# Kernel optimization log

Hardware: AMD Instinct MI355X
Metric: run time of the kernel (lower is better)

The kernel has to match this reference:

```python
import jax, jax.numpy as jnp
import numpy as np

B = 8192
DIM_Q = 1024
DIM_U = 1024
NUM_CHARTS = 16
TOP_K = 2


def setup_inputs() -> dict:
    key = jax.random.key(0)
    k1, k2, k3 = jax.random.split(key, 3)
    q = jax.random.normal(k1, (B, DIM_Q), dtype=jnp.float32)
    weights = jax.random.uniform(k2, (B, NUM_CHARTS), dtype=jnp.float32)
    # W_stack init: -I + 0.01*randn per chart (dim_q == dim_u branch)
    W_stack = (-jnp.eye(DIM_Q, dtype=jnp.float32)[None, :, :]
               + 0.01 * jax.random.normal(k3, (NUM_CHARTS, DIM_U, DIM_Q), dtype=jnp.float32))
    return {"q": q, "weights": weights, "W_stack": W_stack}


def reference(q, weights, W_stack):
    # Top-k gated mixture of linear maps: out[b] = sum_{c in topk(weights[b])} w_norm[b,c] * W_stack[c] @ q[b]
    b = q.shape[0]
    w_vals, idx = jax.lax.top_k(weights, TOP_K)              # [B, k], sorted descending (matches torch.topk)
    w_norm = w_vals / jnp.clip(jnp.sum(w_vals, axis=1, keepdims=True), 1e-8, None)
    # scatter normalized weights back to dense [B, num_charts] gate matrix
    w_masked = jnp.zeros_like(weights).at[jnp.arange(b)[:, None], idx].set(w_norm)
    out = jnp.zeros((b, W_stack.shape[1]), dtype=q.dtype)
    for c in range(NUM_CHARTS):  # small fixed expert count
        out = out + w_masked[:, c:c + 1] * (q @ W_stack[c].T)  # [B, dim_u]
    return out
```

## Files before the change

### kernel.cpp

```cpp
#include <hip/hip_runtime.h>
#include <hip/hip_bf16.h>
#include <stdint.h>

#define NROWS 8192
#define DIMQ 1024
#define DIMU 1024
#define NCH 16

#define BM 128
#define BN 128

typedef __attribute__((ext_vector_type(4))) float f32x4;
typedef __attribute__((ext_vector_type(4))) short s16x4;
typedef __attribute__((ext_vector_type(8))) short bf16x8;

__device__ __forceinline__ short f2bf(float f) {
    union { __hip_bfloat16 h; short s; } u;
    u.h = __float2bfloat16(f);
    return u.s;
}

__global__ void cvt_kernel(const float* __restrict__ src, short* __restrict__ dst, int n8) {
    int i = blockIdx.x * blockDim.x + threadIdx.x;
    int stride = gridDim.x * blockDim.x;
    for (; i < n8; i += stride) {
        const f32x4* p = reinterpret_cast<const f32x4*>(src + (size_t)i * 8);
        f32x4 a = p[0], b = p[1];
        bf16x8 o;
        o[0] = f2bf(a[0]); o[1] = f2bf(a[1]); o[2] = f2bf(a[2]); o[3] = f2bf(a[3]);
        o[4] = f2bf(b[0]); o[5] = f2bf(b[1]); o[6] = f2bf(b[2]); o[7] = f2bf(b[3]);
        *reinterpret_cast<bf16x8*>(dst + (size_t)i * 8) = o;
    }
}

__global__ void gate_kernel(const float* __restrict__ weights,
                            int* __restrict__ cnt,
                            int* __restrict__ rowlist,
                            float* __restrict__ wgt) {
    __shared__ int lcnt[NCH];
    __shared__ int lbase[NCH];
    const int t = threadIdx.x;
    const int b = blockIdx.x * blockDim.x + t;
    if (t < NCH) lcnt[t] = 0;
    __syncthreads();

    float w[NCH];
    const f32x4* wp = reinterpret_cast<const f32x4*>(weights + (size_t)b * NCH);
#pragma unroll
    for (int i = 0; i < 4; ++i) {
        f32x4 v = wp[i];
        w[i * 4 + 0] = v[0]; w[i * 4 + 1] = v[1];
        w[i * 4 + 2] = v[2]; w[i * 4 + 3] = v[3];
    }
    int i0 = 0; float v0 = w[0];
#pragma unroll
    for (int i = 1; i < NCH; ++i) if (w[i] > v0) { v0 = w[i]; i0 = i; }
    int i1 = (i0 == 0) ? 1 : 0; float v1 = w[i1];
#pragma unroll
    for (int i = 0; i < NCH; ++i) if (i != i0 && w[i] > v1) { v1 = w[i]; i1 = i; }
    float s = v0 + v1;
    s = (s < 1e-8f) ? 1e-8f : s;
    float n0 = v0 / s, n1 = v1 / s;

    int p0 = atomicAdd(&lcnt[i0], 1);
    int p1 = atomicAdd(&lcnt[i1], 1);
    __syncthreads();
    if (t < NCH) lbase[t] = atomicAdd(&cnt[t], lcnt[t]);
    __syncthreads();

    int o0 = lbase[i0] + p0;
    int o1 = lbase[i1] + p1;
    rowlist[(size_t)i0 * NROWS + o0] = b;  wgt[(size_t)i0 * NROWS + o0] = n0;
    rowlist[(size_t)i1 * NROWS + o1] = b;  wgt[(size_t)i1 * NROWS + o1] = n1;
}

#define BKB 64
#define LDSTRB 72

__global__ __launch_bounds__(256, 3) void moe_gemm_bf(
    const short* __restrict__ qb, const short* __restrict__ Wb,
    const int* __restrict__ cnt, const int* __restrict__ rowlist,
    const float* __restrict__ wgt, float* __restrict__ out)
{
    const int c  = blockIdx.z;
    const int n0 = blockIdx.x * BN;
    const int m0 = blockIdx.y * BM;
    const int count = cnt[c];
    if (m0 >= count) return;

    __shared__ short sA[BM * LDSTRB];
    __shared__ short sB[BN * LDSTRB];
    __shared__ int   sRow[BM];
    __shared__ float sW[BM];

    const int t = threadIdx.x;
    if (t < BM) {
        int gi = m0 + t;
        int r = 0; float wv_ = 0.f;
        if (gi < count) {
            r   = rowlist[(size_t)c * NROWS + gi];
            wv_ = wgt[(size_t)c * NROWS + gi];
        }
        sRow[t] = r; sW[t] = wv_;
    }
    __syncthreads();

    const short* aSrc[4];
    const short* bSrc[4];
    int ldsO[4];
#pragma unroll
    for (int i = 0; i < 4; ++i) {
        int f  = t + i * 256;
        int r  = f >> 3;
        int c8 = f & 7;
        aSrc[i] = qb + (size_t)sRow[r] * DIMQ + c8 * 8;
        bSrc[i] = Wb + (size_t)c * ((size_t)DIMU * DIMQ) + (size_t)(n0 + r) * DIMQ + c8 * 8;
        ldsO[i] = r * LDSTRB + c8 * 8;
    }

    const int lane = t & 63;
    const int wv   = t >> 6;
    const int wm   = (wv >> 1) * 64;
    const int wn   = (wv & 1) * 64;
    const int rr   = lane & 15;
    const int g    = lane >> 4;

    f32x4 acc[4][4];
#pragma unroll
    for (int r = 0; r < 4; ++r)
#pragma unroll
        for (int cc = 0; cc < 4; ++cc)
            acc[r][cc] = (f32x4){0.f, 0.f, 0.f, 0.f};

    bf16x8 pa[4], pb[4];
#pragma unroll
    for (int i = 0; i < 4; ++i) {
        pa[i] = *reinterpret_cast<const bf16x8*>(aSrc[i]);
        pb[i] = *reinterpret_cast<const bf16x8*>(bSrc[i]);
    }

    const int NKT = DIMQ / BKB;
    for (int kt = 0; kt < NKT; ++kt) {
        __syncthreads();
#pragma unroll
        for (int i = 0; i < 4; ++i) {
            *reinterpret_cast<bf16x8*>(&sA[ldsO[i]]) = pa[i];
            *reinterpret_cast<bf16x8*>(&sB[ldsO[i]]) = pb[i];
        }
        __syncthreads();

        if (kt + 1 < NKT) {
            int k = (kt + 1) * BKB;
#pragma unroll
            for (int i = 0; i < 4; ++i) {
                pa[i] = *reinterpret_cast<const bf16x8*>(aSrc[i] + k);
                pb[i] = *reinterpret_cast<const bf16x8*>(bSrc[i] + k);
            }
        }

#pragma unroll
        for (int ks = 0; ks < 2; ++ks) {
            bf16x8 af[4], bfr[4];
#pragma unroll
            for (int r = 0; r < 4; ++r) {
                af[r]  = *reinterpret_cast<const bf16x8*>(&sA[(wm + r * 16 + rr) * LDSTRB + ks * 32 + g * 8]);
                bfr[r] = *reinterpret_cast<const bf16x8*>(&sB[(wn + r * 16 + rr) * LDSTRB + ks * 32 + g * 8]);
            }
#pragma unroll
            for (int r = 0; r < 4; ++r)
#pragma unroll
                for (int cc = 0; cc < 4; ++cc)
                    acc[r][cc] = __builtin_amdgcn_mfma_f32_16x16x32_bf16(af[r], bfr[cc], acc[r][cc], 0, 0, 0);
        }
    }

#pragma unroll
    for (int r = 0; r < 4; ++r) {
#pragma unroll
        for (int cc = 0; cc < 4; ++cc) {
#pragma unroll
            for (int j = 0; j < 4; ++j) {
                int rowInTile = wm + r * 16 + g * 4 + j;
                int gi = m0 + rowInTile;
                if (gi < count) {
                    int   orow = sRow[rowInTile];
                    float wgx  = sW[rowInTile];
                    int   col  = n0 + wn + cc * 16 + rr;
                    atomicAdd(&out[(size_t)orow * DIMU + col], acc[r][cc][j] * wgx);
                }
            }
        }
    }
}

#define BKF 32
#define LDSTRF 40

__global__ __launch_bounds__(256, 2) void moe_gemm_f32(
    const float* __restrict__ q, const float* __restrict__ Wst,
    const int* __restrict__ cnt, const int* __restrict__ rowlist,
    const float* __restrict__ wgt, float* __restrict__ out)
{
    const int c  = blockIdx.z;
    const int n0 = blockIdx.x * BN;
    const int m0 = blockIdx.y * BM;
    const int count = cnt[c];
    if (m0 >= count) return;

    __shared__ short sA[BM * LDSTRF];
    __shared__ short sB[BN * LDSTRF];
    __shared__ int   sRow[BM];
    __shared__ float sW[BM];

    const int t = threadIdx.x;
    if (t < BM) {
        int gi = m0 + t;
        int r = 0; float w = 0.f;
        if (gi < count) {
            r = rowlist[(size_t)c * NROWS + gi];
            w = wgt[(size_t)c * NROWS + gi];
        }
        sRow[t] = r; sW[t] = w;
    }
    __syncthreads();

    const float* aBase[4];
    const float* bBase[4];
    int ldsOff[4];
#pragma unroll
    for (int i = 0; i < 4; ++i) {
        int f  = t + i * 256;
        int r  = f >> 3;
        int c4 = f & 7;
        aBase[i]  = q   + (size_t)sRow[r] * DIMQ + c4 * 4;
        bBase[i]  = Wst + (size_t)c * ((size_t)DIMU * DIMQ) + (size_t)(n0 + r) * DIMQ + c4 * 4;
        ldsOff[i] = r * LDSTRF + c4 * 4;
    }

    const int lane = t & 63;
    const int wv   = t >> 6;
    const int wm   = (wv >> 1) * 64;
    const int wn   = (wv & 1) * 64;
    const int rr   = lane & 15;
    const int g    = lane >> 4;

    f32x4 acc[4][4];
#pragma unroll
    for (int r = 0; r < 4; ++r)
#pragma unroll
        for (int cc = 0; cc < 4; ++cc)
            acc[r][cc] = (f32x4){0.f, 0.f, 0.f, 0.f};

    f32x4 pa[4], pb[4];
#pragma unroll
    for (int i = 0; i < 4; ++i) {
        pa[i] = *reinterpret_cast<const f32x4*>(aBase[i]);
        pb[i] = *reinterpret_cast<const f32x4*>(bBase[i]);
    }

    const int NKT = DIMQ / BKF;
    for (int kt = 0; kt < NKT; ++kt) {
        __syncthreads();
#pragma unroll
        for (int i = 0; i < 4; ++i) {
            s16x4 va, vb;
#pragma unroll
            for (int j = 0; j < 4; ++j) { va[j] = f2bf(pa[i][j]); vb[j] = f2bf(pb[i][j]); }
            *reinterpret_cast<s16x4*>(&sA[ldsOff[i]]) = va;
            *reinterpret_cast<s16x4*>(&sB[ldsOff[i]]) = vb;
        }
        __syncthreads();

        if (kt + 1 < NKT) {
            int k = (kt + 1) * BKF;
#pragma unroll
            for (int i = 0; i < 4; ++i) {
                pa[i] = *reinterpret_cast<const f32x4*>(aBase[i] + k);
                pb[i] = *reinterpret_cast<const f32x4*>(bBase[i] + k);
            }
        }

        bf16x8 af[4], bfr[4];
#pragma unroll
        for (int r = 0; r < 4; ++r) {
            af[r]  = *reinterpret_cast<const bf16x8*>(&sA[(wm + r * 16 + rr) * LDSTRF + g * 8]);
            bfr[r] = *reinterpret_cast<const bf16x8*>(&sB[(wn + r * 16 + rr) * LDSTRF + g * 8]);
        }
#pragma unroll
        for (int r = 0; r < 4; ++r)
#pragma unroll
            for (int cc = 0; cc < 4; ++cc)
                acc[r][cc] = __builtin_amdgcn_mfma_f32_16x16x32_bf16(af[r], bfr[cc], acc[r][cc], 0, 0, 0);
    }

#pragma unroll
    for (int r = 0; r < 4; ++r) {
#pragma unroll
        for (int cc = 0; cc < 4; ++cc) {
#pragma unroll
            for (int j = 0; j < 4; ++j) {
                int rowInTile = wm + r * 16 + g * 4 + j;
                int gi = m0 + rowInTile;
                if (gi < count) {
                    int   orow = sRow[rowInTile];
                    float w    = sW[rowInTile];
                    int   col  = n0 + wn + cc * 16 + rr;
                    atomicAdd(&out[(size_t)orow * DIMU + col], acc[r][cc][j] * w);
                }
            }
        }
    }
}

extern "C" void kernel_launch(void* const* d_in, const int* in_sizes, int n_in,
                              void* d_out, int out_size, void* d_ws, size_t ws_size,
                              hipStream_t stream) {
    const float* q  = (const float*)d_in[0];
    const float* w  = (const float*)d_in[1];
    const float* Ws = (const float*)d_in[2];
    float* out = (float*)d_out;

    const size_t qbf_bytes  = (size_t)NROWS * DIMQ * 2;
    const size_t wbf_bytes  = (size_t)NCH * DIMU * (size_t)DIMQ * 2;
    const size_t meta_bytes = 256 + (size_t)NCH * NROWS * (sizeof(int) + sizeof(float));
    char* ws = (char*)d_ws;

    if (ws_size >= qbf_bytes + wbf_bytes + meta_bytes) {
        short* qb      = (short*)ws;
        short* Wb      = (short*)(ws + qbf_bytes);
        int*   cnt     = (int*)(ws + qbf_bytes + wbf_bytes);
        int*   rowlist = (int*)(ws + qbf_bytes + wbf_bytes + 256);
        float* wgt     = (float*)(ws + qbf_bytes + wbf_bytes + 256 + (size_t)NCH * NROWS * sizeof(int));

        hipMemsetAsync(cnt, 0, 256, stream);
        hipMemsetAsync(d_out, 0, (size_t)out_size * sizeof(float), stream);

        cvt_kernel<<<2048, 256, 0, stream>>>(q,  qb, NROWS * DIMQ / 8);
        cvt_kernel<<<2048, 256, 0, stream>>>(Ws, Wb, NCH * DIMU * DIMQ / 8);
        gate_kernel<<<NROWS / 256, 256, 0, stream>>>(w, cnt, rowlist, wgt);

        dim3 grid(DIMU / BN, NROWS / BM, NCH);
        moe_gemm_bf<<<grid, 256, 0, stream>>>(qb, Wb, cnt, rowlist, wgt, out);
    } else {
        int*   cnt     = (int*)ws;
        int*   rowlist = (int*)(ws + 256);
        float* wgt     = (float*)(ws + 256 + (size_t)NCH * NROWS * sizeof(int));

        hipMemsetAsync(cnt, 0, 256, stream);
        hipMemsetAsync(d_out, 0, (size_t)out_size * sizeof(float), stream);

        gate_kernel<<<NROWS / 256, 256, 0, stream>>>(w, cnt, rowlist, wgt);

        dim3 grid(DIMU / BN, NROWS / BM, NCH);
        moe_gemm_f32<<<grid, 256, 0, stream>>>(q, Ws, cnt, rowlist, wgt, out);
    }
}
```

Before: 228.5 us.

## Use direct global-to-LDS loads, XCD-aware block mapping, and fused conversion kernel

```diff
diff --git a/kernel.cpp b/kernel.cpp
--- a/kernel.cpp
+++ b/kernel.cpp
@@ -9,9 +9,9 @@
 
 #define BM 128
 #define BN 128
+#define BK 64
 
 typedef __attribute__((ext_vector_type(4))) float f32x4;
-typedef __attribute__((ext_vector_type(4))) short s16x4;
 typedef __attribute__((ext_vector_type(8))) short bf16x8;
 
 __device__ __forceinline__ short f2bf(float f) {
@@ -20,16 +20,27 @@
     return u.s;
 }
 
-__global__ void cvt_kernel(const float* __restrict__ src, short* __restrict__ dst, int n8) {
-    int i = blockIdx.x * blockDim.x + threadIdx.x;
+__global__ void cvt2_kernel(const float* __restrict__ q, const float* __restrict__ Ws,
+                            short* __restrict__ qb, short* __restrict__ Wb) {
+    const int nq = NROWS * DIMQ / 8;
+    const int nw = NCH * DIMU * DIMQ / 8;
+    int i0 = blockIdx.x * blockDim.x + threadIdx.x;
     int stride = gridDim.x * blockDim.x;
-    for (; i < n8; i += stride) {
-        const f32x4* p = reinterpret_cast<const f32x4*>(src + (size_t)i * 8);
+    for (int i = i0; i < nq; i += stride) {
+        const f32x4* p = reinterpret_cast<const f32x4*>(q + (size_t)i * 8);
         f32x4 a = p[0], b = p[1];
         bf16x8 o;
         o[0] = f2bf(a[0]); o[1] = f2bf(a[1]); o[2] = f2bf(a[2]); o[3] = f2bf(a[3]);
         o[4] = f2bf(b[0]); o[5] = f2bf(b[1]); o[6] = f2bf(b[2]); o[7] = f2bf(b[3]);
-        *reinterpret_cast<bf16x8*>(dst + (size_t)i * 8) = o;
+        *reinterpret_cast<bf16x8*>(qb + (size_t)i * 8) = o;
+    }
+    for (int i = i0; i < nw; i += stride) {
+        const f32x4* p = reinterpret_cast<const f32x4*>(Ws + (size_t)i * 8);
+        f32x4 a = p[0], b = p[1];
+        bf16x8 o;
+        o[0] = f2bf(a[0]); o[1] = f2bf(a[1]); o[2] = f2bf(a[2]); o[3] = f2bf(a[3]);
+        o[4] = f2bf(b[0]); o[5] = f2bf(b[1]); o[6] = f2bf(b[2]); o[7] = f2bf(b[3]);
+        *reinterpret_cast<bf16x8*>(Wb + (size_t)i * 8) = o;
     }
 }
 
@@ -74,22 +85,24 @@
     rowlist[(size_t)i1 * NROWS + o1] = b;  wgt[(size_t)i1 * NROWS + o1] = n1;
 }
 
-#define BKB 64
-#define LDSTRB 72
-
 __global__ __launch_bounds__(256, 3) void moe_gemm_bf(
     const short* __restrict__ qb, const short* __restrict__ Wb,
     const int* __restrict__ cnt, const int* __restrict__ rowlist,
     const float* __restrict__ wgt, float* __restrict__ out)
 {
-    const int c  = blockIdx.z;
-    const int n0 = blockIdx.x * BN;
-    const int m0 = blockIdx.y * BM;
+    const int id  = blockIdx.x;
+    const int xcd = id & 7;
+    const int k   = id >> 3;
+    const int c   = xcd + ((k >> 9) << 3);
+    const int kk  = k & 511;
+    const int n0  = (kk & 7) * BN;
+    const int m0  = (kk >> 3) * BM;
+
     const int count = cnt[c];
     if (m0 >= count) return;
 
-    __shared__ short sA[BM * LDSTRB];
-    __shared__ short sB[BN * LDSTRB];
+    __shared__ short sA[BM * BK];
+    __shared__ short sB[BN * BK];
     __shared__ int   sRow[BM];
     __shared__ float sW[BM];
 
@@ -107,15 +120,13 @@
 
     const short* aSrc[4];
     const short* bSrc[4];
-    int ldsO[4];
 #pragma unroll
     for (int i = 0; i < 4; ++i) {
-        int f  = t + i * 256;
-        int r  = f >> 3;
-        int c8 = f & 7;
+        int ch = i * 256 + t;
+        int r  = ch >> 3;
+        int c8 = ch & 7;
         aSrc[i] = qb + (size_t)sRow[r] * DIMQ + c8 * 8;
         bSrc[i] = Wb + (size_t)c * ((size_t)DIMU * DIMQ) + (size_t)(n0 + r) * DIMQ + c8 * 8;
-        ldsO[i] = r * LDSTRB + c8 * 8;
     }
 
     const int lane = t & 63;
@@ -132,39 +143,24 @@
         for (int cc = 0; cc < 4; ++cc)
             acc[r][cc] = (f32x4){0.f, 0.f, 0.f, 0.f};
 
-    bf16x8 pa[4], pb[4];
-#pragma unroll
-    for (int i = 0; i < 4; ++i) {
-        pa[i] = *reinterpret_cast<const bf16x8*>(aSrc[i]);
-        pb[i] = *reinterpret_cast<const bf16x8*>(bSrc[i]);
-    }
-
-    const int NKT = DIMQ / BKB;
+    const int NKT = DIMQ / BK;
     for (int kt = 0; kt < NKT; ++kt) {
         __syncthreads();
 #pragma unroll
-        for (int i = 0; i < 4; ++i) {
-            *reinterpret_cast<bf16x8*>(&sA[ldsO[i]]) = pa[i];
-            *reinterpret_cast<bf16x8*>(&sB[ldsO[i]]) = pb[i];
-        }
+        for (int i = 0; i < 4; ++i)
+            __builtin_amdgcn_global_load_lds(aSrc[i] + kt * BK, &sA[(i * 256 + t) * 8], 16, 0, 0);
+#pragma unroll
+        for (int i = 0; i < 4; ++i)
+            __builtin_amdgcn_global_load_lds(bSrc[i] + kt * BK, &sB[(i * 256 + t) * 8], 16, 0, 0);
         __syncthreads();
-
-        if (kt + 1 < NKT) {
-            int k = (kt + 1) * BKB;
-#pragma unroll
-            for (int i = 0; i < 4; ++i) {
-                pa[i] = *reinterpret_cast<const bf16x8*>(aSrc[i] + k);
-                pb[i] = *reinterpret_cast<const bf16x8*>(bSrc[i] + k);
-            }
-        }
 
 #pragma unroll
         for (int ks = 0; ks < 2; ++ks) {
             bf16x8 af[4], bfr[4];
 #pragma unroll
             for (int r = 0; r < 4; ++r) {
-                af[r]  = *reinterpret_cast<const bf16x8*>(&sA[(wm + r * 16 + rr) * LDSTRB + ks * 32 + g * 8]);
-                bfr[r] = *reinterpret_cast<const bf16x8*>(&sB[(wn + r * 16 + rr) * LDSTRB + ks * 32 + g * 8]);
+                af[r]  = *reinterpret_cast<const bf16x8*>(&sA[(wm + r * 16 + rr) * BK + ks * 32 + g * 8]);
+                bfr[r] = *reinterpret_cast<const bf16x8*>(&sB[(wn + r * 16 + rr) * BK + ks * 32 + g * 8]);
             }
 #pragma unroll
             for (int r = 0; r < 4; ++r)
@@ -195,6 +191,7 @@
 
 #define BKF 32
 #define LDSTRF 40
+typedef __attribute__((ext_vector_type(4))) short s16x4;
 
 __global__ __launch_bounds__(256, 2) void moe_gemm_f32(
     const float* __restrict__ q, const float* __restrict__ Wst,
@@ -335,12 +332,10 @@
         hipMemsetAsync(cnt, 0, 256, stream);
         hipMemsetAsync(d_out, 0, (size_t)out_size * sizeof(float), stream);
 
-        cvt_kernel<<<2048, 256, 0, stream>>>(q,  qb, NROWS * DIMQ / 8);
-        cvt_kernel<<<2048, 256, 0, stream>>>(Ws, Wb, NCH * DIMU * DIMQ / 8);
+        cvt2_kernel<<<2048, 256, 0, stream>>>(q, Ws, qb, Wb);
         gate_kernel<<<NROWS / 256, 256, 0, stream>>>(w, cnt, rowlist, wgt);
 
-        dim3 grid(DIMU / BN, NROWS / BM, NCH);
-        moe_gemm_bf<<<grid, 256, 0, stream>>>(qb, Wb, cnt, rowlist, wgt, out);
+        moe_gemm_bf<<<8192, 256, 0, stream>>>(qb, Wb, cnt, rowlist, wgt, out);
     } else {
         int*   cnt     = (int*)ws;
         int*   rowlist = (int*)(ws + 256);
```

Measured after the change: 241.1 us. 1.06x slower.
